# Optimization experiments

Hardware: AMD Instinct MI355X
Metric: run time of the kernel (lower is better)

The kernel has to match this reference:

```python
import jax, jax.numpy as jnp
import numpy as np

N = 100000   # nodes
E = 1600000  # edges
D = 128      # in_dim == hidden_dim (residual-friendly)
C = 47       # num_classes
EPS = 1e-5   # BatchNorm eps


def _glorot(key, shape):
    fan = shape[0] + shape[1]
    return jax.random.uniform(key, shape, jnp.float32, -1.0, 1.0) * np.sqrt(6.0 / fan)


def setup_inputs() -> dict:
    key = jax.random.key(0)
    ks = jax.random.split(key, 16)
    inp = {
        "x": jax.random.normal(ks[0], (N, D), jnp.float32),
        "edge_index": jax.random.randint(ks[1], (2, E), 0, N, jnp.int32),
    }
    # Per-layer SAGEConv params: lin_l (root, with bias) and lin_r (neighbor, no bias)
    for i, k in zip((1, 2, 3), (ks[2], ks[3], ks[4])):
        k1, k2 = jax.random.split(k)
        inp[f"Wl{i}"] = _glorot(k1, (D, D))
        inp[f"bl{i}"] = jnp.zeros((D,), jnp.float32)
        inp[f"Wr{i}"] = _glorot(k2, (D, D))
        inp[f"bn_g{i}"] = jnp.ones((D,), jnp.float32)
        inp[f"bn_b{i}"] = jnp.zeros((D,), jnp.float32)
    inp["lin_W"] = _glorot(ks[5], (C, D))
    inp["lin_b"] = jnp.zeros((C,), jnp.float32)
    return inp


def _sage_conv(x, src, dst, Wl, bl, Wr):
    # mean aggregation of source features at destination nodes
    msg = jax.ops.segment_sum(x[src], dst, num_segments=N)            # [N, D]
    cnt = jax.ops.segment_sum(jnp.ones((src.shape[0],), x.dtype), dst, num_segments=N)
    mean = msg / jnp.maximum(cnt, 1.0)[:, None]
    return x @ Wl.T + bl + mean @ Wr.T


def _batch_norm(h, g, b):
    mu = h.mean(axis=0)
    var = h.var(axis=0)
    return (h - mu) * jax.lax.rsqrt(var + EPS) * g + b


def reference(x, edge_index,
              Wl1, bl1, Wr1, bn_g1, bn_b1,
              Wl2, bl2, Wr2, bn_g2, bn_b2,
              Wl3, bl3, Wr3, bn_g3, bn_b3,
              lin_W, lin_b):
    src, dst = edge_index[0], edge_index[1]
    layers = [(Wl1, bl1, Wr1, bn_g1, bn_b1),
              (Wl2, bl2, Wr2, bn_g2, bn_b2),
              (Wl3, bl3, Wr3, bn_g3, bn_b3)]
    for Wl, bl, Wr, g, b in layers:
        h = _sage_conv(x, src, dst, Wl, bl, Wr)
        h = jax.nn.relu(_batch_norm(h, g, b))
        # dropout is identity in deterministic/eval reference
        x = x + h  # shapes always match since in_dim == hidden_dim
    return x @ lin_W.T + lin_b
```

## Files before the change

kernel.cpp:

```cpp
#include <hip/hip_runtime.h>

typedef __attribute__((ext_vector_type(8))) short short8;
typedef __attribute__((ext_vector_type(4))) float f32x4;
typedef __attribute__((ext_vector_type(2))) float f32x2;

constexpr int NN = 100000;
constexpr int EE = 1600000;
constexpr int DD = 128;
constexpr int CC = 47;
constexpr int NB = 391;
constexpr int BSLOT = 5120;
constexpr int GB = 782;

constexpr size_t OFF_XB   = 0;
constexpr size_t OFF_MB   = 25600000;
constexpr size_t OFF_HB   = 51200000;
constexpr size_t OFF_XQ   = 76800000;
constexpr size_t OFF_BIN  = 89600000;
constexpr size_t OFF_CSR  = 97607680;
constexpr size_t OFF_RP   = 104007680;
constexpr size_t OFF_CUR  = 104407808;
constexpr size_t OFF_W    = 104411904;
constexpr size_t OFF_ST   = 104620800;

static __device__ __forceinline__ float bf2f(unsigned short u) {
    return __uint_as_float(((unsigned)u) << 16);
}
static __device__ __forceinline__ unsigned short f2bf(float f) {
    unsigned u = __float_as_uint(f);
    unsigned r = (u + 0x7fffu + ((u >> 16) & 1u)) >> 16;
    return (unsigned short)r;
}
static __device__ __forceinline__ uint2 pack8_fp8(const float* f) {
    int w0 = 0, w1 = 0;
    w0 = __builtin_amdgcn_cvt_pk_fp8_f32(f[0], f[1], w0, false);
    w0 = __builtin_amdgcn_cvt_pk_fp8_f32(f[2], f[3], w0, true);
    w1 = __builtin_amdgcn_cvt_pk_fp8_f32(f[4], f[5], w1, false);
    w1 = __builtin_amdgcn_cvt_pk_fp8_f32(f[6], f[7], w1, true);
    return uint2{(unsigned)w0, (unsigned)w1};
}

__global__ void k_prep(const float* __restrict__ wl1, const float* __restrict__ wr1,
                       const float* __restrict__ wl2, const float* __restrict__ wr2,
                       const float* __restrict__ wl3, const float* __restrict__ wr3,
                       const float* __restrict__ lw, unsigned short* __restrict__ wdst,
                       const float* __restrict__ x, unsigned short* __restrict__ xb,
                       unsigned char* __restrict__ xq, int* __restrict__ cur) {
    int bid = blockIdx.x;
    int id = bid * 256 + threadIdx.x;
    if (id < NB) cur[id] = 0;
    if (bid < 408) {
        if (id < 98304) {
            int L = id >> 15;
            int r = id & 32767;
            int mat = r >> 14;
            int t = r & 16383;
            int j = t & 7, lane = (t >> 3) & 63, ct = (t >> 9) & 7, ks = t >> 12;
            int row = ct * 16 + (lane & 15);
            int col = ks * 32 + ((lane >> 4) << 3) + j;
            const float* src = (L == 0) ? (mat ? wr1 : wl1)
                             : (L == 1) ? (mat ? wr2 : wl2)
                                        : (mat ? wr3 : wl3);
            wdst[id] = f2bf(src[row * 128 + col]);
        } else if (id < 98304 + 6144) {
            int t = id - 98304;
            int j = t & 7, lane = (t >> 3) & 63, m = t >> 9;
            int ct = m % 3, ks = m / 3;
            int row = ct * 16 + (lane & 15);
            int col = ks * 32 + ((lane >> 4) << 3) + j;
            wdst[id] = (row < CC) ? f2bf(lw[row * 128 + col]) : (unsigned short)0;
        }
    } else {
        int i = ((bid - 408) * 256 + threadIdx.x) * 8;
        if (i >= NN * DD) return;
        float4 v1 = *(const float4*)(x + i);
        float4 v2 = *(const float4*)(x + i + 4);
        float f[8] = {v1.x, v1.y, v1.z, v1.w, v2.x, v2.y, v2.z, v2.w};
        short8 o;
        #pragma unroll
        for (int j = 0; j < 8; ++j) o[j] = (short)f2bf(f[j]);
        *(short8*)(xb + i) = o;
        *(uint2*)(xq + i) = pack8_fp8(f);
    }
}

__global__ __launch_bounds__(256) void k_bin(const int* __restrict__ ei,
                                             int* __restrict__ cur, int* __restrict__ bin) {
    __shared__ int cnt[NB];
    int t = threadIdx.x;
    for (int b = t; b < NB; b += 256) cnt[b] = 0;
    __syncthreads();
    int start = blockIdx.x * 3125;
    for (int i = t; i < 3125; i += 256) {
        int d = ei[EE + start + i];
        atomicAdd(&cnt[d >> 8], 1);
    }
    __syncthreads();
    int c[2], b0[2];
    #pragma unroll
    for (int k = 0; k < 2; ++k) {
        int b = t + k * 256;
        if (b < NB) { c[k] = cnt[b]; b0[k] = (c[k] > 0) ? atomicAdd(&cur[b], c[k]) : 0; }
    }
    __syncthreads();
    #pragma unroll
    for (int k = 0; k < 2; ++k) {
        int b = t + k * 256;
        if (b < NB) cnt[b] = b0[k];
    }
    __syncthreads();
    for (int i = t; i < 3125; i += 256) {
        int s = ei[start + i];
        int d = ei[EE + start + i];
        int b = d >> 8;
        int p = atomicAdd(&cnt[b], 1);
        if (p < BSLOT) bin[b * BSLOT + p] = (s << 8) | (d & 255);
    }
}

__global__ __launch_bounds__(256) void k_build(const int* __restrict__ cur,
                                               int* __restrict__ rp, const int* __restrict__ bin,
                                               int* __restrict__ csr) {
    __shared__ int lcnt[256], lsc[256], lrun[256], red[256];
    int b = blockIdx.x, t = threadIdx.x;
    int partial = 0;
    for (int i = t; i < b; i += 256) partial += cur[i];
    red[t] = partial;
    __syncthreads();
    for (int off = 128; off > 0; off >>= 1) {
        if (t < off) red[t] += red[t + off];
        __syncthreads();
    }
    int bb = red[0];
    __syncthreads();
    if (b == NB - 1 && t == 0) rp[NN] = bb + cur[b];

    int n0 = b << 8;
    int nodes = NN - n0; if (nodes > 256) nodes = 256;
    int tot = cur[b]; if (tot > BSLOT) tot = BSLOT;
    lcnt[t] = 0;
    __syncthreads();
    const int* bsrc = bin + b * BSLOT;
    for (int i = t; i < tot; i += 256) atomicAdd(&lcnt[bsrc[i] & 255], 1);
    __syncthreads();
    int c = lcnt[t];
    lsc[t] = c;
    __syncthreads();
    for (int off = 1; off < 256; off <<= 1) {
        int v = (t >= off) ? lsc[t - off] : 0;
        __syncthreads();
        lsc[t] += v;
        __syncthreads();
    }
    int excl = lsc[t] - c;
    if (t < nodes) rp[n0 + t] = bb + excl;
    lrun[t] = bb + excl;
    __syncthreads();
    for (int i = t; i < tot; i += 256) {
        int v = bsrc[i];
        int p = atomicAdd(&lrun[v & 255], 1);
        csr[p] = (v >> 8) << 7;
    }
}

__global__ __launch_bounds__(256) void k_agg(const int* __restrict__ rp, const int* __restrict__ csr,
                                             const unsigned char* __restrict__ xq,
                                             unsigned short* __restrict__ mb,
                                             float* __restrict__ st) {
    if (blockIdx.x == 0) st[threadIdx.x] = 0.f;
    int node = blockIdx.x * 4 + (threadIdx.x >> 6);
    if (node >= NN) return;
    int lane = threadIdx.x & 63;
    int g = lane >> 4;
    int cb = (lane & 15) << 3;
    int s0 = rp[node], s1 = rp[node + 1];
    int deg = s1 - s0;
    f32x2 acc0 = {0.f, 0.f}, acc1 = {0.f, 0.f}, acc2 = {0.f, 0.f}, acc3 = {0.f, 0.f};
    int nb = deg >> 4;
    int e = s0 + g;
    for (int k = 0; k < nb; ++k) {
        int i0 = csr[e];
        int i1 = csr[e + 4];
        int i2 = csr[e + 8];
        int i3 = csr[e + 12];
        uint2 v0 = *(const uint2*)(xq + i0 + cb);
        uint2 v1 = *(const uint2*)(xq + i1 + cb);
        uint2 v2 = *(const uint2*)(xq + i2 + cb);
        uint2 v3 = *(const uint2*)(xq + i3 + cb);
        acc0 += __builtin_amdgcn_cvt_pk_f32_fp8(v0.x, false);
        acc1 += __builtin_amdgcn_cvt_pk_f32_fp8(v0.x, true);
        acc2 += __builtin_amdgcn_cvt_pk_f32_fp8(v0.y, false);
        acc3 += __builtin_amdgcn_cvt_pk_f32_fp8(v0.y, true);
        acc0 += __builtin_amdgcn_cvt_pk_f32_fp8(v1.x, false);
        acc1 += __builtin_amdgcn_cvt_pk_f32_fp8(v1.x, true);
        acc2 += __builtin_amdgcn_cvt_pk_f32_fp8(v1.y, false);
        acc3 += __builtin_amdgcn_cvt_pk_f32_fp8(v1.y, true);
        acc0 += __builtin_amdgcn_cvt_pk_f32_fp8(v2.x, false);
        acc1 += __builtin_amdgcn_cvt_pk_f32_fp8(v2.x, true);
        acc2 += __builtin_amdgcn_cvt_pk_f32_fp8(v2.y, false);
        acc3 += __builtin_amdgcn_cvt_pk_f32_fp8(v2.y, true);
        acc0 += __builtin_amdgcn_cvt_pk_f32_fp8(v3.x, false);
        acc1 += __builtin_amdgcn_cvt_pk_f32_fp8(v3.x, true);
        acc2 += __builtin_amdgcn_cvt_pk_f32_fp8(v3.y, false);
        acc3 += __builtin_amdgcn_cvt_pk_f32_fp8(v3.y, true);
        e += 16;
    }
    for (; e < s1; e += 4) {
        int i0 = csr[e];
        uint2 v0 = *(const uint2*)(xq + i0 + cb);
        acc0 += __builtin_amdgcn_cvt_pk_f32_fp8(v0.x, false);
        acc1 += __builtin_amdgcn_cvt_pk_f32_fp8(v0.x, true);
        acc2 += __builtin_amdgcn_cvt_pk_f32_fp8(v0.y, false);
        acc3 += __builtin_amdgcn_cvt_pk_f32_fp8(v0.y, true);
    }
    float acc[8] = {acc0[0], acc0[1], acc1[0], acc1[1],
                    acc2[0], acc2[1], acc3[0], acc3[1]};
    #pragma unroll
    for (int j = 0; j < 8; ++j) {
        acc[j] += __shfl_xor(acc[j], 16);
        acc[j] += __shfl_xor(acc[j], 32);
    }
    if (g == 0) {
        float inv = 1.0f / (float)(deg > 1 ? deg : 1);
        short8 o;
        #pragma unroll
        for (int j = 0; j < 8; ++j) o[j] = (short)f2bf(acc[j] * inv);
        *(short8*)(mb + (size_t)node * 128 + cb) = o;
    }
}

__global__ __launch_bounds__(512, 6) void k_gemm(const unsigned short* __restrict__ xb,
                                                 const unsigned short* __restrict__ mb,
                                                 const unsigned short* __restrict__ wf,
                                                 const float* __restrict__ bias,
                                                 unsigned short* __restrict__ hb,
                                                 float* __restrict__ st) {
    __shared__ unsigned short wsh[16384];
    __shared__ float rbuf[2048];
    int tid = threadIdx.x;
    int wave = tid >> 6, lane = tid & 63, q = lane >> 4, l15 = lane & 15;
    int rowbase = blockIdx.x * 128 + wave * 16;
    int arow = rowbase + l15;

    f32x4 acc[8];
    #pragma unroll
    for (int ct = 0; ct < 8; ++ct) {
        float bv = bias[ct * 16 + l15];
        f32x4 t = {bv, bv, bv, bv};
        acc[ct] = t;
    }

    #pragma unroll
    for (int mat = 0; mat < 2; ++mat) {
        const unsigned short* src = mat ? mb : xb;
        const int4* wsrc = (const int4*)(wf + (mat << 14));
        if (mat) __syncthreads();
        #pragma unroll
        for (int i = 0; i < 4; ++i)
            ((int4*)wsh)[tid + i * 512] = wsrc[tid + i * 512];
        __syncthreads();
        #pragma unroll
        for (int ks = 0; ks < 4; ++ks) {
            short8 a;
            if (arow < NN) a = *(const short8*)(src + (size_t)arow * 128 + ks * 32 + (q << 3));
            else           a = short8{0,0,0,0,0,0,0,0};
            #pragma unroll
            for (int ct = 0; ct < 8; ++ct) {
                short8 b = *(const short8*)(wsh + ((ks * 8 + ct) << 9) + (lane << 3));
                acc[ct] = __builtin_amdgcn_mfma_f32_16x16x32_bf16(a, b, acc[ct], 0, 0, 0);
            }
        }
    }

    #pragma unroll
    for (int ct = 0; ct < 8; ++ct) {
        int colg = ct * 16 + l15;
        float sv = 0.f, qv = 0.f;
        #pragma unroll
        for (int r = 0; r < 4; ++r) {
            int row = rowbase + (q << 2) + r;
            if (row < NN) {
                float v = acc[ct][r];
                hb[(size_t)row * 128 + colg] = f2bf(v);
                sv += v; qv += v * v;
            }
        }
        sv += __shfl_xor(sv, 16); sv += __shfl_xor(sv, 32);
        qv += __shfl_xor(qv, 16); qv += __shfl_xor(qv, 32);
        if (q == 0) {
            rbuf[wave * 256 + colg] = sv;
            rbuf[wave * 256 + 128 + colg] = qv;
        }
    }
    __syncthreads();
    if (tid < 256) {
        float v = 0.f;
        #pragma unroll
        for (int w = 0; w < 8; ++w) v += rbuf[w * 256 + tid];
        atomicAdd(&st[tid], v);
    }
}

__global__ void k_bn(const unsigned short* __restrict__ hb,
                     const float* __restrict__ stats, const float* __restrict__ gam,
                     const float* __restrict__ bet, unsigned short* __restrict__ xb,
                     unsigned char* __restrict__ xq) {
    int i = (blockIdx.x * 256 + threadIdx.x) * 8;
    if (i >= NN * DD) return;
    int col = i & 127;
    const float invN = 1.0f / (float)NN;
    short8 hv = *(const short8*)(hb + i);
    short8 xv = *(const short8*)(xb + i);
    short8 o;
    float f[8];
    #pragma unroll
    for (int j = 0; j < 8; ++j) {
        int c = col + j;
        float mu = stats[c] * invN;
        float var = stats[128 + c] * invN - mu * mu;
        float sc = rsqrtf(var + 1e-5f) * gam[c];
        float val = (bf2f((unsigned short)hv[j]) - mu) * sc + bet[c];
        float r = bf2f((unsigned short)xv[j]) + (val > 0.f ? val : 0.f);
        f[j] = r;
        o[j] = (short)f2bf(r);
    }
    *(short8*)(xb + i) = o;
    *(uint2*)(xq + i) = pack8_fp8(f);
}

__global__ __launch_bounds__(256) void k_final(const unsigned short* __restrict__ xb,
                                               const unsigned short* __restrict__ wf,
                                               const float* __restrict__ bias,
                                               float* __restrict__ out) {
    __shared__ unsigned short wsh[6144];
    int tid = threadIdx.x;
    #pragma unroll
    for (int i = 0; i < 3; ++i) {
        int idx = tid + i * 256;
        if (idx < 768) ((int4*)wsh)[idx] = ((const int4*)wf)[idx];
    }
    __syncthreads();

    int wave = tid >> 6, lane = tid & 63, q = lane >> 4, l15 = lane & 15;
    int rowbase = blockIdx.x * 256 + wave * 64;

    f32x4 acc[4][3];
    #pragma unroll
    for (int ct = 0; ct < 3; ++ct) {
        int colg = ct * 16 + l15;
        float bv = (colg < CC) ? bias[colg] : 0.f;
        f32x4 t = {bv, bv, bv, bv};
        #pragma unroll
        for (int rt = 0; rt < 4; ++rt) acc[rt][ct] = t;
    }
    #pragma unroll
    for (int ks = 0; ks < 4; ++ks) {
        short8 a[4];
        #pragma unroll
        for (int rt = 0; rt < 4; ++rt) {
            int row = rowbase + rt * 16 + l15;
            if (row < NN) a[rt] = *(const short8*)(xb + (size_t)row * 128 + ks * 32 + (q << 3));
            else          a[rt] = short8{0,0,0,0,0,0,0,0};
        }
        #pragma unroll
        for (int ct = 0; ct < 3; ++ct) {
            short8 b = *(const short8*)(wsh + ((ks * 3 + ct) << 9) + (lane << 3));
            #pragma unroll
            for (int rt = 0; rt < 4; ++rt)
                acc[rt][ct] = __builtin_amdgcn_mfma_f32_16x16x32_bf16(a[rt], b, acc[rt][ct], 0, 0, 0);
        }
    }
    #pragma unroll
    for (int ct = 0; ct < 3; ++ct) {
        int colg = ct * 16 + l15;
        if (colg >= CC) continue;
        #pragma unroll
        for (int rt = 0; rt < 4; ++rt) {
            #pragma unroll
            for (int r = 0; r < 4; ++r) {
                int row = rowbase + rt * 16 + (q << 2) + r;
                if (row < NN) out[(size_t)row * CC + colg] = acc[rt][ct][r];
            }
        }
    }
}

extern "C" void kernel_launch(void* const* d_in, const int* in_sizes, int n_in,
                              void* d_out, int out_size, void* d_ws, size_t ws_size,
                              hipStream_t stream) {
    const float* x   = (const float*)d_in[0];
    const int*   ei  = (const int*)d_in[1];
    const float* Wl[3]  = {(const float*)d_in[2],  (const float*)d_in[7],  (const float*)d_in[12]};
    const float* bl[3]  = {(const float*)d_in[3],  (const float*)d_in[8],  (const float*)d_in[13]};
    const float* Wr[3]  = {(const float*)d_in[4],  (const float*)d_in[9],  (const float*)d_in[14]};
    const float* bng[3] = {(const float*)d_in[5],  (const float*)d_in[10], (const float*)d_in[15]};
    const float* bnb[3] = {(const float*)d_in[6],  (const float*)d_in[11], (const float*)d_in[16]};
    const float* linW = (const float*)d_in[17];
    const float* linb = (const float*)d_in[18];

    char* ws = (char*)d_ws;
    unsigned short* xb   = (unsigned short*)(ws + OFF_XB);
    unsigned short* mb   = (unsigned short*)(ws + OFF_MB);
    unsigned short* hb   = (unsigned short*)(ws + OFF_HB);
    unsigned char*  xq   = (unsigned char*)(ws + OFF_XQ);
    int*            bin  = (int*)(ws + OFF_BIN);
    int*            csr  = (int*)(ws + OFF_CSR);
    int*            rp   = (int*)(ws + OFF_RP);
    int*            cur  = (int*)(ws + OFF_CUR);
    unsigned short* wfr  = (unsigned short*)(ws + OFF_W);
    float*          st   = (float*)(ws + OFF_ST);

    k_prep<<<6658, 256, 0, stream>>>(Wl[0], Wr[0], Wl[1], Wr[1], Wl[2], Wr[2], linW, wfr,
                                     x, xb, xq, cur);
    k_bin<<<512, 256, 0, stream>>>(ei, cur, bin);
    k_build<<<NB, 256, 0, stream>>>(cur, rp, bin, csr);

    for (int l = 0; l < 3; ++l) {
        const unsigned short* wfp = wfr + (size_t)l * 32768;
        k_agg<<<25000, 256, 0, stream>>>(rp, csr, xq, mb, st);
        k_gemm<<<GB, 512, 0, stream>>>(xb, mb, wfp, bl[l], hb, st);
        k_bn<<<6250, 256, 0, stream>>>(hb, st, bng[l], bnb[l], xb, xq);
    }
    k_final<<<391, 256, 0, stream>>>(xb, wfr + 98304, linb, (float*)d_out);
}
```

Baseline: 480.3 us.

## Fuse last-layer BatchNorm into final classifier and prefetch second GEMM operands

The last layer's BN+ReLU+residual is fused into the final linear kernel. The updated rows are staged in shared memory, so the bf16 x write/read and the fp8 copy for the third layer are no longer produced. In k_gemm, all A-row fragments for both operands and the second weight matrix are loaded into registers up front, so global latency overlaps the first MFMA pass. The cost is higher register pressure in k_gemm and more shared memory per block in the final kernel.

After: 491.9 us. 1.02x slower.

```diff
diff --git a/kernel.cpp b/kernel.cpp
--- a/kernel.cpp
+++ b/kernel.cpp
@@ -241,6 +241,7 @@
     int wave = tid >> 6, lane = tid & 63, q = lane >> 4, l15 = lane & 15;
     int rowbase = blockIdx.x * 128 + wave * 16;
     int arow = rowbase + l15;
+    bool rowok = arow < NN;
 
     f32x4 acc[8];
     #pragma unroll
@@ -251,24 +252,44 @@
     }
 
     #pragma unroll
-    for (int mat = 0; mat < 2; ++mat) {
-        const unsigned short* src = mat ? mb : xb;
-        const int4* wsrc = (const int4*)(wf + (mat << 14));
-        if (mat) __syncthreads();
-        #pragma unroll
-        for (int i = 0; i < 4; ++i)
-            ((int4*)wsh)[tid + i * 512] = wsrc[tid + i * 512];
-        __syncthreads();
-        #pragma unroll
-        for (int ks = 0; ks < 4; ++ks) {
-            short8 a;
-            if (arow < NN) a = *(const short8*)(src + (size_t)arow * 128 + ks * 32 + (q << 3));
-            else           a = short8{0,0,0,0,0,0,0,0};
-            #pragma unroll
-            for (int ct = 0; ct < 8; ++ct) {
-                short8 b = *(const short8*)(wsh + ((ks * 8 + ct) << 9) + (lane << 3));
-                acc[ct] = __builtin_amdgcn_mfma_f32_16x16x32_bf16(a, b, acc[ct], 0, 0, 0);
-            }
+    for (int i = 0; i < 4; ++i)
+        ((int4*)wsh)[tid + i * 512] = ((const int4*)wf)[tid + i * 512];
+    short8 a0[4];
+    #pragma unroll
+    for (int ks = 0; ks < 4; ++ks)
+        a0[ks] = rowok ? *(const short8*)(xb + (size_t)arow * 128 + ks * 32 + (q << 3))
+                       : short8{0,0,0,0,0,0,0,0};
+    __syncthreads();
+
+    int4 w1[4];
+    #pragma unroll
+    for (int i = 0; i < 4; ++i)
+        w1[i] = ((const int4*)(wf + 16384))[tid + i * 512];
+    short8 a1[4];
+    #pragma unroll
+    for (int ks = 0; ks < 4; ++ks)
+        a1[ks] = rowok ? *(const short8*)(mb + (size_t)arow * 128 + ks * 32 + (q << 3))
+                       : short8{0,0,0,0,0,0,0,0};
+
+    #pragma unroll
+    for (int ks = 0; ks < 4; ++ks) {
+        #pragma unroll
+        for (int ct = 0; ct < 8; ++ct) {
+            short8 b = *(const short8*)(wsh + ((ks * 8 + ct) << 9) + (lane << 3));
+            acc[ct] = __builtin_amdgcn_mfma_f32_16x16x32_bf16(a0[ks], b, acc[ct], 0, 0, 0);
+        }
+    }
+    __syncthreads();
+    #pragma unroll
+    for (int i = 0; i < 4; ++i)
+        ((int4*)wsh)[tid + i * 512] = w1[i];
+    __syncthreads();
+    #pragma unroll
+    for (int ks = 0; ks < 4; ++ks) {
+        #pragma unroll
+        for (int ct = 0; ct < 8; ++ct) {
+            short8 b = *(const short8*)(wsh + ((ks * 8 + ct) << 9) + (lane << 3));
+            acc[ct] = __builtin_amdgcn_mfma_f32_16x16x32_bf16(a1[ks], b, acc[ct], 0, 0, 0);
         }
     }
 
@@ -328,10 +349,15 @@
     *(uint2*)(xq + i) = pack8_fp8(f);
 }
 
-__global__ __launch_bounds__(256) void k_final(const unsigned short* __restrict__ xb,
-                                               const unsigned short* __restrict__ wf,
-                                               const float* __restrict__ bias,
-                                               float* __restrict__ out) {
+__global__ __launch_bounds__(256) void k_bnfinal(const unsigned short* __restrict__ hb,
+                                                 const unsigned short* __restrict__ xb,
+                                                 const float* __restrict__ stats,
+                                                 const float* __restrict__ gam,
+                                                 const float* __restrict__ bet,
+                                                 const unsigned short* __restrict__ wf,
+                                                 const float* __restrict__ bias,
+                                                 float* __restrict__ out) {
+    __shared__ unsigned short xt[128 * 132];
     __shared__ unsigned short wsh[6144];
     int tid = threadIdx.x;
     #pragma unroll
@@ -339,34 +365,55 @@
         int idx = tid + i * 256;
         if (idx < 768) ((int4*)wsh)[idx] = ((const int4*)wf)[idx];
     }
+
+    int rowb0 = blockIdx.x * 128;
+    const float invN = 1.0f / (float)NN;
+    #pragma unroll
+    for (int it = 0; it < 8; ++it) {
+        int ch = tid + it * 256;
+        int lrow = ch >> 4, seg = ch & 15;
+        int grow = rowb0 + lrow;
+        short8 o = short8{0,0,0,0,0,0,0,0};
+        if (grow < NN) {
+            short8 hv = *(const short8*)(hb + (size_t)grow * 128 + seg * 8);
+            short8 xv = *(const short8*)(xb + (size_t)grow * 128 + seg * 8);
+            #pragma unroll
+            for (int j = 0; j < 8; ++j) {
+                int c = seg * 8 + j;
+                float mu = stats[c] * invN;
+                float var = stats[128 + c] * invN - mu * mu;
+                float sc = rsqrtf(var + 1e-5f) * gam[c];
+                float val = (bf2f((unsigned short)hv[j]) - mu) * sc + bet[c];
+                float r = bf2f((unsigned short)xv[j]) + (val > 0.f ? val : 0.f);
+                o[j] = (short)f2bf(r);
+            }
+        }
+        *(short8*)(xt + lrow * 132 + seg * 8) = o;
+    }
     __syncthreads();
 
     int wave = tid >> 6, lane = tid & 63, q = lane >> 4, l15 = lane & 15;
-    int rowbase = blockIdx.x * 256 + wave * 64;
-
-    f32x4 acc[4][3];
+    int lrow0 = wave * 32;
+
+    f32x4 acc[2][3];
     #pragma unroll
     for (int ct = 0; ct < 3; ++ct) {
         int colg = ct * 16 + l15;
         float bv = (colg < CC) ? bias[colg] : 0.f;
         f32x4 t = {bv, bv, bv, bv};
-        #pragma unroll
-        for (int rt = 0; rt < 4; ++rt) acc[rt][ct] = t;
+        acc[0][ct] = t; acc[1][ct] = t;
     }
     #pragma unroll
     for (int ks = 0; ks < 4; ++ks) {
-        short8 a[4];
-        #pragma unroll
-        for (int rt = 0; rt < 4; ++rt) {
-            int row = rowbase + rt * 16 + l15;
-            if (row < NN) a[rt] = *(const short8*)(xb + (size_t)row * 128 + ks * 32 + (q << 3));
-            else          a[rt] = short8{0,0,0,0,0,0,0,0};
-        }
+        short8 a[2];
+        #pragma unroll
+        for (int rt = 0; rt < 2; ++rt)
+            a[rt] = *(const short8*)(xt + (lrow0 + rt * 16 + l15) * 132 + ks * 32 + (q << 3));
         #pragma unroll
         for (int ct = 0; ct < 3; ++ct) {
             short8 b = *(const short8*)(wsh + ((ks * 3 + ct) << 9) + (lane << 3));
             #pragma unroll
-            for (int rt = 0; rt < 4; ++rt)
+            for (int rt = 0; rt < 2; ++rt)
                 acc[rt][ct] = __builtin_amdgcn_mfma_f32_16x16x32_bf16(a[rt], b, acc[rt][ct], 0, 0, 0);
         }
     }
@@ -375,10 +422,10 @@
         int colg = ct * 16 + l15;
         if (colg >= CC) continue;
         #pragma unroll
-        for (int rt = 0; rt < 4; ++rt) {
+        for (int rt = 0; rt < 2; ++rt) {
             #pragma unroll
             for (int r = 0; r < 4; ++r) {
-                int row = rowbase + rt * 16 + (q << 2) + r;
+                int row = rowb0 + lrow0 + rt * 16 + (q << 2) + r;
                 if (row < NN) out[(size_t)row * CC + colg] = acc[rt][ct][r];
             }
         }
@@ -419,7 +466,9 @@
         const unsigned short* wfp = wfr + (size_t)l * 32768;
         k_agg<<<25000, 256, 0, stream>>>(rp, csr, xq, mb, st);
         k_gemm<<<GB, 512, 0, stream>>>(xb, mb, wfp, bl[l], hb, st);
-        k_bn<<<6250, 256, 0, stream>>>(hb, st, bng[l], bnb[l], xb, xq);
-    }
-    k_final<<<391, 256, 0, stream>>>(xb, wfr + 98304, linb, (float*)d_out);
-}
+        if (l < 2)
+            k_bn<<<6250, 256, 0, stream>>>(hb, st, bng[l], bnb[l], xb, xq);
+    }
+    k_bnfinal<<<GB, 256, 0, stream>>>(hb, xb, st, bng[2], bnb[2], wfr + 98304, linb,
+                                      (float*)d_out);
+}
```
